# Kernel optimization log

Measured on AMD Instinct MI355X. Metric: run time of the kernel, lower is better.

The kernel has to match this reference:

```python
import jax, jax.numpy as jnp
import numpy as np

SPATIAL = 8  # spatial_size


def setup_inputs() -> dict:
    key = jax.random.key(0)
    k1, k2 = jax.random.split(key)
    B, C, T, H, W = 8, 1, 16, 500, 500
    inp = jax.random.normal(k1, (B, C, T, H, W), dtype=jnp.float32)
    stdv = 1.0 / np.sqrt(T)  # matches reset_parameters scaling
    weight = jax.random.uniform(k2, (T, 4, 4), dtype=jnp.float32, minval=-stdv, maxval=stdv)
    return {"input": inp, "weight": weight, "pad_h": 512, "pad_w": 512,
            "n_patch_h": 127, "n_patch_w": 127}


def reference(input, weight, pad_h, pad_w, n_patch_h, n_patch_w):
    B, C, T, H, W = input.shape
    step = weight.shape[1]  # spatial_size // 2 (overlapping)
    s = SPATIAL

    # zero-pad bottom/right to the padded frame size
    x = jnp.pad(input, ((0, 0), (0, 0), (0, 0), (0, pad_h - H), (0, pad_w - W)))

    # weight.repeat(B, C, 1, n_patch_h+1, n_patch_w+1): tile step-blocks over frame;
    # broadcast over (B, C) instead of materializing the full repeat.
    w_tiled = jnp.tile(weight, (1, n_patch_h + 1, n_patch_w + 1))  # (T, pad_h, pad_w)

    # masked multiply + temporal sum -> coded snapshot (B, C, pad_h, pad_w)
    output = jnp.einsum('bcthw,thw->bchw', x, w_tiled)

    # overlapping patch extraction: unfold(2, s, step).unfold(3, s, step)
    hh = (jnp.arange(n_patch_h) * step)[:, None] + jnp.arange(s)  # (nph, s)
    ww = (jnp.arange(n_patch_w) * step)[:, None] + jnp.arange(s)  # (npw, s)
    patches = output[:, :, hh[:, None, :, None], ww[None, :, None, :]]  # (B,C,nph,npw,s,s)

    # permute(0,1,2,3,5,4) then flatten to (B, C*nph*npw, s*s)
    patches = jnp.swapaxes(patches, -1, -2)
    patches = patches.reshape(B, -1, s * s)

    return patches, output[:, :, :H, :W]
```

## Files before the change

kernel.cpp:

```cpp
#include <hip/hip_runtime.h>

#define B_DIM 8
#define T_DIM 16
#define H_IN 500
#define W_IN 500
#define HP 512
#define WP 512
#define NPH 127
#define NPW 127
#define STEP 4
#define SP 8
#define LDS_STRIDE 516

__global__ __launch_bounds__(256) void k_conv(const float* __restrict__ in,
                                              const float* __restrict__ wgt,
                                              float* __restrict__ ws,
                                              float* __restrict__ crop) {
    __shared__ float4 wlds[T_DIM * 4];
    int tid = threadIdx.x;
    if (tid < T_DIM * 4) wlds[tid] = reinterpret_cast<const float4*>(wgt)[tid];
    __syncthreads();

    int idx = blockIdx.x * 256 + tid;
    int w4  = idx & 127;
    int h   = (idx >> 7) & 511;
    int b   = idx >> 16;
    int w0  = w4 * 4;

    float4 acc = {0.f, 0.f, 0.f, 0.f};
    bool valid = (h < H_IN) && (w0 < W_IN);
    if (valid) {
        const float* base = in + (size_t)b * T_DIM * (H_IN * W_IN) + h * W_IN + w0;
        int hr = h & 3;
        #pragma unroll
        for (int t = 0; t < T_DIM; ++t) {
            float4 xv = *reinterpret_cast<const float4*>(base + (size_t)t * (H_IN * W_IN));
            float4 wv = wlds[t * 4 + hr];
            acc.x += xv.x * wv.x;
            acc.y += xv.y * wv.y;
            acc.z += xv.z * wv.z;
            acc.w += xv.w * wv.w;
        }
    }
    reinterpret_cast<float4*>(ws)[idx] = acc;
    if (valid) {
        *reinterpret_cast<float4*>(crop + ((size_t)b * H_IN + h) * W_IN + w0) = acc;
    }
}

__global__ __launch_bounds__(256) void k_patch(const float* __restrict__ ws,
                                               float* __restrict__ patches) {
    __shared__ float lds[SP * LDS_STRIDE];
    int blk = blockIdx.x;
    int ph  = blk % NPH;
    int b   = blk / NPH;
    int tid = threadIdx.x;

    const float* src = ws + ((size_t)b * HP + ph * STEP) * WP;
    #pragma unroll
    for (int k = 0; k < 4; ++k) {
        int e = tid + k * 256;
        int r = e >> 7;
        int c = (e & 127) * 4;
        float4 v = *reinterpret_cast<const float4*>(src + r * WP + c);
        *reinterpret_cast<float4*>(&lds[r * LDS_STRIDE + c]) = v;
    }
    __syncthreads();

    float* dst = patches + ((size_t)b * NPH * NPW + (size_t)ph * NPW) * 64;
    for (int e4 = tid; e4 < NPW * 16; e4 += 256) {
        int i0 = (e4 & 1) * 4;
        int j  = (e4 >> 1) & 7;
        int pw = e4 >> 4;
        float4 v;
        v.x = lds[(i0 + 0) * LDS_STRIDE + pw * 4 + j];
        v.y = lds[(i0 + 1) * LDS_STRIDE + pw * 4 + j];
        v.z = lds[(i0 + 2) * LDS_STRIDE + pw * 4 + j];
        v.w = lds[(i0 + 3) * LDS_STRIDE + pw * 4 + j];
        reinterpret_cast<float4*>(dst)[e4] = v;
    }
}

__global__ __launch_bounds__(256) void k_fused(const float* __restrict__ in,
                                               const float* __restrict__ wgt,
                                               float* __restrict__ patches,
                                               float* __restrict__ crop) {
    __shared__ float lds[SP * LDS_STRIDE];
    __shared__ float4 wlds[T_DIM * 4];
    int tid = threadIdx.x;
    if (tid < T_DIM * 4) wlds[tid] = reinterpret_cast<const float4*>(wgt)[tid];
    __syncthreads();

    int blk = blockIdx.x;
    int ph  = blk % NPH;
    int b   = blk / NPH;

    #pragma unroll
    for (int k = 0; k < 4; ++k) {
        int e = tid + k * 256;
        int r = e >> 7;
        int c = (e & 127) * 4;
        int h = ph * STEP + r;
        float4 acc = {0.f, 0.f, 0.f, 0.f};
        if (h < H_IN && c < W_IN) {
            const float* base = in + (size_t)b * T_DIM * (H_IN * W_IN) + h * W_IN + c;
            int hr = h & 3;
            #pragma unroll
            for (int t = 0; t < T_DIM; ++t) {
                float4 xv = *reinterpret_cast<const float4*>(base + (size_t)t * (H_IN * W_IN));
                float4 wv = wlds[t * 4 + hr];
                acc.x += xv.x * wv.x;
                acc.y += xv.y * wv.y;
                acc.z += xv.z * wv.z;
                acc.w += xv.w * wv.w;
            }
            *reinterpret_cast<float4*>(crop + ((size_t)b * H_IN + h) * W_IN + c) = acc;
        }
        *reinterpret_cast<float4*>(&lds[r * LDS_STRIDE + c]) = acc;
    }
    __syncthreads();

    float* dst = patches + ((size_t)b * NPH * NPW + (size_t)ph * NPW) * 64;
    for (int e4 = tid; e4 < NPW * 16; e4 += 256) {
        int i0 = (e4 & 1) * 4;
        int j  = (e4 >> 1) & 7;
        int pw = e4 >> 4;
        float4 v;
        v.x = lds[(i0 + 0) * LDS_STRIDE + pw * 4 + j];
        v.y = lds[(i0 + 1) * LDS_STRIDE + pw * 4 + j];
        v.z = lds[(i0 + 2) * LDS_STRIDE + pw * 4 + j];
        v.w = lds[(i0 + 3) * LDS_STRIDE + pw * 4 + j];
        reinterpret_cast<float4*>(dst)[e4] = v;
    }
}

extern "C" void kernel_launch(void* const* d_in, const int* in_sizes, int n_in,
                              void* d_out, int out_size, void* d_ws, size_t ws_size,
                              hipStream_t stream) {
    const float* in  = (const float*)d_in[0];
    const float* wgt = (const float*)d_in[1];
    float* out     = (float*)d_out;
    float* patches = out;
    float* crop    = out + (size_t)B_DIM * NPH * NPW * 64;

    size_t ws_need = (size_t)B_DIM * HP * WP * sizeof(float);
    if (ws_size >= ws_need) {
        float* ws = (float*)d_ws;
        k_conv <<<(B_DIM * HP * (WP / 4)) / 256, 256, 0, stream>>>(in, wgt, ws, crop);
        k_patch<<<B_DIM * NPH, 256, 0, stream>>>(ws, patches);
    } else {
        k_fused<<<B_DIM * NPH, 256, 0, stream>>>(in, wgt, patches, crop);
    }
}
```

Baseline: 35.99 us.

## Fuse conv and patch extraction into non-overlapping 8-row band kernel

Replaces the two-kernel path (conv to a workspace, then patch extraction) with a single kernel where each block computes a non-overlapping 8-row band of the coded snapshot once. Each band writes a full patch row plus the lower and upper halves of the two neighbouring overlapping patch rows. This removes the workspace write and re-read and avoids the 2x recomputation of the old fused fallback. Block indices are also swizzled across batches to spread work. In exchange, the half-row patch stores become strided, with each block writing interleaved float4s.

Measured after the change: 30.49 us. -15.3%, faster.

```diff
diff --git a/kernel.cpp b/kernel.cpp
--- a/kernel.cpp
+++ b/kernel.cpp
@@ -4,103 +4,32 @@
 #define T_DIM 16
 #define H_IN 500
 #define W_IN 500
-#define HP 512
-#define WP 512
 #define NPH 127
 #define NPW 127
 #define STEP 4
-#define SP 8
-#define LDS_STRIDE 516
+#define LSTR 516
 
-__global__ __launch_bounds__(256) void k_conv(const float* __restrict__ in,
+__global__ __launch_bounds__(256) void k_band(const float* __restrict__ in,
                                               const float* __restrict__ wgt,
-                                              float* __restrict__ ws,
+                                              float* __restrict__ patches,
                                               float* __restrict__ crop) {
+    __shared__ float lds[8 * LSTR];
     __shared__ float4 wlds[T_DIM * 4];
     int tid = threadIdx.x;
     if (tid < T_DIM * 4) wlds[tid] = reinterpret_cast<const float4*>(wgt)[tid];
+
+    int orig = blockIdx.x;
+    int n = (orig & 7) * 64 + (orig >> 3);
+    int q = n & 63;
+    int b = n >> 6;
     __syncthreads();
-
-    int idx = blockIdx.x * 256 + tid;
-    int w4  = idx & 127;
-    int h   = (idx >> 7) & 511;
-    int b   = idx >> 16;
-    int w0  = w4 * 4;
-
-    float4 acc = {0.f, 0.f, 0.f, 0.f};
-    bool valid = (h < H_IN) && (w0 < W_IN);
-    if (valid) {
-        const float* base = in + (size_t)b * T_DIM * (H_IN * W_IN) + h * W_IN + w0;
-        int hr = h & 3;
-        #pragma unroll
-        for (int t = 0; t < T_DIM; ++t) {
-            float4 xv = *reinterpret_cast<const float4*>(base + (size_t)t * (H_IN * W_IN));
-            float4 wv = wlds[t * 4 + hr];
-            acc.x += xv.x * wv.x;
-            acc.y += xv.y * wv.y;
-            acc.z += xv.z * wv.z;
-            acc.w += xv.w * wv.w;
-        }
-    }
-    reinterpret_cast<float4*>(ws)[idx] = acc;
-    if (valid) {
-        *reinterpret_cast<float4*>(crop + ((size_t)b * H_IN + h) * W_IN + w0) = acc;
-    }
-}
-
-__global__ __launch_bounds__(256) void k_patch(const float* __restrict__ ws,
-                                               float* __restrict__ patches) {
-    __shared__ float lds[SP * LDS_STRIDE];
-    int blk = blockIdx.x;
-    int ph  = blk % NPH;
-    int b   = blk / NPH;
-    int tid = threadIdx.x;
-
-    const float* src = ws + ((size_t)b * HP + ph * STEP) * WP;
-    #pragma unroll
-    for (int k = 0; k < 4; ++k) {
-        int e = tid + k * 256;
-        int r = e >> 7;
-        int c = (e & 127) * 4;
-        float4 v = *reinterpret_cast<const float4*>(src + r * WP + c);
-        *reinterpret_cast<float4*>(&lds[r * LDS_STRIDE + c]) = v;
-    }
-    __syncthreads();
-
-    float* dst = patches + ((size_t)b * NPH * NPW + (size_t)ph * NPW) * 64;
-    for (int e4 = tid; e4 < NPW * 16; e4 += 256) {
-        int i0 = (e4 & 1) * 4;
-        int j  = (e4 >> 1) & 7;
-        int pw = e4 >> 4;
-        float4 v;
-        v.x = lds[(i0 + 0) * LDS_STRIDE + pw * 4 + j];
-        v.y = lds[(i0 + 1) * LDS_STRIDE + pw * 4 + j];
-        v.z = lds[(i0 + 2) * LDS_STRIDE + pw * 4 + j];
-        v.w = lds[(i0 + 3) * LDS_STRIDE + pw * 4 + j];
-        reinterpret_cast<float4*>(dst)[e4] = v;
-    }
-}
-
-__global__ __launch_bounds__(256) void k_fused(const float* __restrict__ in,
-                                               const float* __restrict__ wgt,
-                                               float* __restrict__ patches,
-                                               float* __restrict__ crop) {
-    __shared__ float lds[SP * LDS_STRIDE];
-    __shared__ float4 wlds[T_DIM * 4];
-    int tid = threadIdx.x;
-    if (tid < T_DIM * 4) wlds[tid] = reinterpret_cast<const float4*>(wgt)[tid];
-    __syncthreads();
-
-    int blk = blockIdx.x;
-    int ph  = blk % NPH;
-    int b   = blk / NPH;
 
     #pragma unroll
     for (int k = 0; k < 4; ++k) {
         int e = tid + k * 256;
         int r = e >> 7;
         int c = (e & 127) * 4;
-        int h = ph * STEP + r;
+        int h = q * 8 + r;
         float4 acc = {0.f, 0.f, 0.f, 0.f};
         if (h < H_IN && c < W_IN) {
             const float* base = in + (size_t)b * T_DIM * (H_IN * W_IN) + h * W_IN + c;
@@ -116,21 +45,52 @@
             }
             *reinterpret_cast<float4*>(crop + ((size_t)b * H_IN + h) * W_IN + c) = acc;
         }
-        *reinterpret_cast<float4*>(&lds[r * LDS_STRIDE + c]) = acc;
+        *reinterpret_cast<float4*>(&lds[r * LSTR + c]) = acc;
     }
     __syncthreads();
 
-    float* dst = patches + ((size_t)b * NPH * NPW + (size_t)ph * NPW) * 64;
-    for (int e4 = tid; e4 < NPW * 16; e4 += 256) {
-        int i0 = (e4 & 1) * 4;
-        int j  = (e4 >> 1) & 7;
-        int pw = e4 >> 4;
-        float4 v;
-        v.x = lds[(i0 + 0) * LDS_STRIDE + pw * 4 + j];
-        v.y = lds[(i0 + 1) * LDS_STRIDE + pw * 4 + j];
-        v.z = lds[(i0 + 2) * LDS_STRIDE + pw * 4 + j];
-        v.w = lds[(i0 + 3) * LDS_STRIDE + pw * 4 + j];
-        reinterpret_cast<float4*>(dst)[e4] = v;
+    {
+        float* dst = patches + (((size_t)b * NPH + 2 * q) * NPW) * 64;
+        for (int e4 = tid; e4 < NPW * 16; e4 += 256) {
+            int i0 = (e4 & 1) * 4;
+            int j  = (e4 >> 1) & 7;
+            int pw = e4 >> 4;
+            int col = pw * STEP + j;
+            float4 v;
+            v.x = lds[(i0 + 0) * LSTR + col];
+            v.y = lds[(i0 + 1) * LSTR + col];
+            v.z = lds[(i0 + 2) * LSTR + col];
+            v.w = lds[(i0 + 3) * LSTR + col];
+            reinterpret_cast<float4*>(dst)[e4] = v;
+        }
+    }
+    if (q < 63) {
+        float* dst = patches + (((size_t)b * NPH + 2 * q + 1) * NPW) * 64;
+        for (int e = tid; e < NPW * 8; e += 256) {
+            int j  = e & 7;
+            int pw = e >> 3;
+            int col = pw * STEP + j;
+            float4 v;
+            v.x = lds[4 * LSTR + col];
+            v.y = lds[5 * LSTR + col];
+            v.z = lds[6 * LSTR + col];
+            v.w = lds[7 * LSTR + col];
+            reinterpret_cast<float4*>(dst)[pw * 16 + j * 2] = v;
+        }
+    }
+    if (q > 0) {
+        float* dst = patches + (((size_t)b * NPH + 2 * q - 1) * NPW) * 64;
+        for (int e = tid; e < NPW * 8; e += 256) {
+            int j  = e & 7;
+            int pw = e >> 3;
+            int col = pw * STEP + j;
+            float4 v;
+            v.x = lds[0 * LSTR + col];
+            v.y = lds[1 * LSTR + col];
+            v.z = lds[2 * LSTR + col];
+            v.w = lds[3 * LSTR + col];
+            reinterpret_cast<float4*>(dst)[pw * 16 + j * 2 + 1] = v;
+        }
     }
 }
 
@@ -143,12 +103,5 @@
     float* patches = out;
     float* crop    = out + (size_t)B_DIM * NPH * NPW * 64;
 
-    size_t ws_need = (size_t)B_DIM * HP * WP * sizeof(float);
-    if (ws_size >= ws_need) {
-        float* ws = (float*)d_ws;
-        k_conv <<<(B_DIM * HP * (WP / 4)) / 256, 256, 0, stream>>>(in, wgt, ws, crop);
-        k_patch<<<B_DIM * NPH, 256, 0, stream>>>(ws, patches);
-    } else {
-        k_fused<<<B_DIM * NPH, 256, 0, stream>>>(in, wgt, patches, crop);
-    }
+    k_band<<<B_DIM * 64, 256, 0, stream>>>(in, wgt, patches, crop);
 }
```
